# Performance work log

Measured on AMD Instinct MI355X. Metric: run time of the kernel, lower is better.

Reference implementation:

```python
import jax, jax.numpy as jnp
import numpy as np

B, S, D, H = 4, 2048, 256, 8
HD = D // H  # 32
SCALE = 1.0 / jnp.sqrt(256.0)  # module divides by sqrt(256.0), NOT sqrt(head_dim)


def setup_inputs() -> dict:
    key = jax.random.key(0)
    ks = jax.random.split(key, 11)
    inp = {
        "q_in": jax.random.normal(ks[0], (B, S, D), jnp.float32),
        "k_in": jax.random.normal(ks[1], (B, S, D), jnp.float32),
        "v_in": jax.random.normal(ks[2], (B, S, D), jnp.float32),
        # causal mask, broadcastable over batch and heads; every row has >=1 one
        "mask": jnp.tril(jnp.ones((S, S), jnp.float32))[None, None, :, :],
        "Wq": jax.random.normal(ks[3], (D, D), jnp.float32) * 0.05,
        "bq": jnp.zeros((D,), jnp.float32),
        "Wk": jax.random.normal(ks[4], (D, D), jnp.float32) * 0.05,
        "bk": jnp.zeros((D,), jnp.float32),
        "Wv": jax.random.normal(ks[5], (D, D), jnp.float32) * 0.05,
        "bv": jnp.zeros((D,), jnp.float32),
        "Wo": jax.random.normal(ks[6], (D, D), jnp.float32) * 0.05,
        "bo": jnp.zeros((D,), jnp.float32),
    }
    return inp


def _mask_softmax(x, mask):
    # faithful to module: exp (no max-subtraction), remask, normalize
    e = jnp.exp(x) * mask
    return e / jnp.sum(e, axis=-1, keepdims=True)


def reference(q_in, k_in, v_in, mask, Wq, bq, Wk, bk, Wv, bv, Wo, bo):
    Q = (q_in @ Wq + bq).reshape(B, S, H, HD)
    K = (k_in @ Wk + bk).reshape(B, S, H, HD)
    V = (v_in @ Wv + bv).reshape(B, S, H, HD)
    scores = jnp.einsum("bqhd,bkhd->bhqk", Q, K) * SCALE  # [B,H,S,S]
    scores = scores * mask  # module multiplies mask into scores first
    p = _mask_softmax(scores, mask)
    attn = jnp.einsum("bhqk,bkhd->bqhd", p, V).reshape(B, S, D)
    return attn @ Wo + bo
```

## Files before the change

kernel.cpp:

```cpp
#include <hip/hip_runtime.h>
#include <hip/hip_bf16.h>

#define BATCH 4
#define S_LEN 2048
#define D_MOD 256
#define NH 8
#define HDIM 32
#define SCALE_ 0.0625f

typedef short bf16x8 __attribute__((ext_vector_type(8)));
typedef short short4v __attribute__((ext_vector_type(4)));
typedef float f32x4 __attribute__((ext_vector_type(4)));

__device__ __forceinline__ short f2bf(float f) {
    __hip_bfloat16 h = __float2bfloat16(f);
    return *reinterpret_cast<short*>(&h);
}

__global__ __launch_bounds__(256) void wtrans_kernel(
    const float* __restrict__ Wq, const float* __restrict__ Wk,
    const float* __restrict__ Wv, const float* __restrict__ Wo,
    short* __restrict__ WT)
{
    const int wsel = blockIdx.x;
    const int k0 = blockIdx.y * 8;
    const float* W = wsel == 0 ? Wq : (wsel == 1 ? Wk : (wsel == 2 ? Wv : Wo));
    short* T = WT + (size_t)wsel * 256 * 256;
    int n = threadIdx.x;
    bf16x8 o;
    #pragma unroll
    for (int kk = 0; kk < 8; ++kk)
        o[kk] = f2bf(W[(size_t)(k0 + kk) * 256 + n]);
    *(bf16x8*)&T[(size_t)n * 256 + k0] = o;
}

__global__ __launch_bounds__(256) void qkv_proj_kernel(
    const float* __restrict__ q_in, const float* __restrict__ k_in,
    const float* __restrict__ v_in, const short* __restrict__ WT,
    const float* __restrict__ bq, const float* __restrict__ bk,
    const float* __restrict__ bv,
    short* __restrict__ Qp, short* __restrict__ Kp, short* __restrict__ Vt)
{
    __shared__ short lsA[32][264];
    const int mt = blockIdx.x;
    const int seg = blockIdx.y;
    const float* A = seg == 0 ? q_in : (seg == 1 ? k_in : v_in);
    const short* WTs = WT + (size_t)seg * 65536;
    const float* bias = seg == 0 ? bq : (seg == 1 ? bk : bv);
    const int m0 = mt * 32;
    const int tid = threadIdx.x;

    {
        const float4* A4 = (const float4*)(A + (size_t)m0 * D_MOD);
        #pragma unroll
        for (int i = 0; i < 8; ++i) {
            int f4 = tid + i * 256;
            int row = f4 >> 6, c4 = f4 & 63;
            float4 v = A4[f4];
            short4v o;
            o.x = f2bf(v.x); o.y = f2bf(v.y); o.z = f2bf(v.z); o.w = f2bf(v.w);
            *(short4v*)&lsA[row][c4 * 4] = o;
        }
    }
    __syncthreads();

    const int w = tid >> 6, l = tid & 63, g = l >> 4, r15 = l & 15;
    bf16x8 af[2][8];
    #pragma unroll
    for (int f = 0; f < 2; ++f)
        #pragma unroll
        for (int kk = 0; kk < 8; ++kk)
            af[f][kk] = *(const bf16x8*)&lsA[f * 16 + r15][kk * 32 + 8 * g];

    const int bidx = m0 >> 11;
    const int s_base = m0 & (S_LEN - 1);

    #pragma unroll
    for (int ntl = 0; ntl < 4; ++ntl) {
        int col = w * 64 + ntl * 16 + r15;
        f32x4 acc0 = {}, acc1 = {};
        #pragma unroll
        for (int kk = 0; kk < 8; ++kk) {
            bf16x8 b = *(const bf16x8*)&WTs[(size_t)col * 256 + kk * 32 + 8 * g];
            acc0 = __builtin_amdgcn_mfma_f32_16x16x32_bf16(af[0][kk], b, acc0, 0, 0, 0);
            acc1 = __builtin_amdgcn_mfma_f32_16x16x32_bf16(af[1][kk], b, acc1, 0, 0, 0);
        }
        float bval = bias[col];
        int h = col >> 5, hd = col & 31;
        if (seg < 2) {
            short* Out = seg == 0 ? Qp : Kp;
            short* Outh = Out + ((size_t)(bidx * NH + h) * S_LEN) * HDIM;
            #pragma unroll
            for (int r = 0; r < 4; ++r) {
                int s0 = s_base + 4 * g + r;
                Outh[(size_t)s0 * HDIM + hd]        = f2bf(acc0[r] + bval);
                Outh[(size_t)(s0 + 16) * HDIM + hd] = f2bf(acc1[r] + bval);
            }
        } else {
            short* Vh = Vt + ((size_t)(bidx * NH + h) * HDIM + hd) * S_LEN;
            short4v o0, o1;
            #pragma unroll
            for (int r = 0; r < 4; ++r) { o0[r] = f2bf(acc0[r] + bval); o1[r] = f2bf(acc1[r] + bval); }
            size_t s = s_base + 4 * g;
            *(short4v*)&Vh[s]      = o0;
            *(short4v*)&Vh[s + 16] = o1;
        }
    }
}

__global__ __launch_bounds__(256) void attn_kernel(
    const short* __restrict__ Qp, const short* __restrict__ Kp,
    const short* __restrict__ Vt, short* __restrict__ Ab)
{
    __shared__ char smem[18432];
    __shared__ float psl[4][2][16];
    short (*pl)[32][72] = (short(*)[32][72])smem;
    float (*comb)[32][33] = (float(*)[32][33])smem;

    const int idx = blockIdx.x;
    const int bh = 4 * (idx & 7) + ((idx >> 3) & 3);
    const int jq = idx >> 5;
    const int b = bh >> 3, h = bh & 7;
    const int tid = threadIdx.x;
    const int w = tid >> 6, l = tid & 63, g = l >> 4, r15 = l & 15;
    const int q0 = jq * 32;

    const short* Qph = Qp + (size_t)bh * S_LEN * HDIM;
    const short* Kph = Kp + (size_t)bh * S_LEN * HDIM;
    const short* Vtp = Vt + (size_t)bh * HDIM * S_LEN;

    bf16x8 aq0 = *(const bf16x8*)&Qph[(size_t)(q0 + r15) * HDIM + 8 * g];
    bf16x8 aq1 = *(const bf16x8*)&Qph[(size_t)(q0 + 16 + r15) * HDIM + 8 * g];

    f32x4 oacc[2][2] = {};
    float ps0[4] = {}, ps1[4] = {};
    const f32x4 zero = {};
    const int ntiles = (q0 + 95) >> 6;

    for (int kt = w; kt < ntiles; kt += 4) {
        const int k0 = kt * 64;
        const bool full = (k0 + 63) <= q0;
        #pragma unroll
        for (int n = 0; n < 4; ++n) {
            bf16x8 bk = *(const bf16x8*)&Kph[(size_t)(k0 + n * 16 + r15) * HDIM + 8 * g];
            f32x4 s0 = __builtin_amdgcn_mfma_f32_16x16x32_bf16(aq0, bk, zero, 0, 0, 0);
            f32x4 s1 = __builtin_amdgcn_mfma_f32_16x16x32_bf16(aq1, bk, zero, 0, 0, 0);
            int key = k0 + n * 16 + r15;
            if (full) {
                #pragma unroll
                for (int r = 0; r < 4; ++r) {
                    float e0 = __expf(s0[r] * SCALE_);
                    float e1 = __expf(s1[r] * SCALE_);
                    ps0[r] += e0; ps1[r] += e1;
                    pl[w][4 * g + r][n * 16 + r15]      = f2bf(e0);
                    pl[w][16 + 4 * g + r][n * 16 + r15] = f2bf(e1);
                }
            } else {
                #pragma unroll
                for (int r = 0; r < 4; ++r) {
                    int qr = q0 + 4 * g + r;
                    float e0 = (key <= qr)      ? __expf(s0[r] * SCALE_) : 0.0f;
                    float e1 = (key <= qr + 16) ? __expf(s1[r] * SCALE_) : 0.0f;
                    ps0[r] += e0; ps1[r] += e1;
                    pl[w][4 * g + r][n * 16 + r15]      = f2bf(e0);
                    pl[w][16 + 4 * g + r][n * 16 + r15] = f2bf(e1);
                }
            }
        }
        #pragma unroll
        for (int ks = 0; ks < 2; ++ks) {
            bf16x8 pa0 = *(const bf16x8*)&pl[w][r15][ks * 32 + 8 * g];
            bf16x8 pa1 = *(const bf16x8*)&pl[w][16 + r15][ks * 32 + 8 * g];
            #pragma unroll
            for (int n2 = 0; n2 < 2; ++n2) {
                bf16x8 bv = *(const bf16x8*)&Vtp[(size_t)(n2 * 16 + r15) * S_LEN + k0 + ks * 32 + 8 * g];
                oacc[0][n2] = __builtin_amdgcn_mfma_f32_16x16x32_bf16(pa0, bv, oacc[0][n2], 0, 0, 0);
                oacc[1][n2] = __builtin_amdgcn_mfma_f32_16x16x32_bf16(pa1, bv, oacc[1][n2], 0, 0, 0);
            }
        }
    }

    #pragma unroll
    for (int r = 0; r < 4; ++r) {
        float v0 = ps0[r], v1 = ps1[r];
        v0 += __shfl_xor(v0, 1); v1 += __shfl_xor(v1, 1);
        v0 += __shfl_xor(v0, 2); v1 += __shfl_xor(v1, 2);
        v0 += __shfl_xor(v0, 4); v1 += __shfl_xor(v1, 4);
        v0 += __shfl_xor(v0, 8); v1 += __shfl_xor(v1, 8);
        ps0[r] = v0; ps1[r] = v1;
    }

    __syncthreads();
    #pragma unroll
    for (int n2 = 0; n2 < 2; ++n2) {
        #pragma unroll
        for (int r = 0; r < 4; ++r) {
            comb[w][4 * g + r][n2 * 16 + r15]      = oacc[0][n2][r];
            comb[w][16 + 4 * g + r][n2 * 16 + r15] = oacc[1][n2][r];
        }
    }
    if (r15 == 0) {
        #pragma unroll
        for (int r = 0; r < 4; ++r) {
            psl[w][0][4 * g + r] = ps0[r];
            psl[w][1][4 * g + r] = ps1[r];
        }
    }
    __syncthreads();

    {
        int q = tid >> 3, hd0 = (tid & 7) * 4;
        int qf = q >> 4, q15 = q & 15;
        float ps = psl[0][qf][q15] + psl[1][qf][q15] + psl[2][qf][q15] + psl[3][qf][q15];
        float inv = __fdividef(1.0f, ps);
        short4v o;
        #pragma unroll
        for (int j = 0; j < 4; ++j) {
            float v = comb[0][q][hd0 + j] + comb[1][q][hd0 + j]
                    + comb[2][q][hd0 + j] + comb[3][q][hd0 + j];
            o[j] = f2bf(v * inv);
        }
        *(short4v*)&Ab[((size_t)b * S_LEN + q0 + q) * D_MOD + h * HDIM + hd0] = o;
    }
}

__global__ __launch_bounds__(256) void out_proj_kernel(
    const short* __restrict__ Ab, const short* __restrict__ WTo,
    const float* __restrict__ bo, float* __restrict__ out)
{
    const int m0 = blockIdx.x * 32;
    const int tid = threadIdx.x;
    const int w = tid >> 6, l = tid & 63, g = l >> 4, r15 = l & 15;

    bf16x8 af[2][8];
    #pragma unroll
    for (int f = 0; f < 2; ++f)
        #pragma unroll
        for (int kk = 0; kk < 8; ++kk)
            af[f][kk] = *(const bf16x8*)&Ab[(size_t)(m0 + f * 16 + r15) * D_MOD + kk * 32 + 8 * g];

    #pragma unroll
    for (int ntl = 0; ntl < 4; ++ntl) {
        int col = w * 64 + ntl * 16 + r15;
        f32x4 acc0 = {}, acc1 = {};
        #pragma unroll
        for (int kk = 0; kk < 8; ++kk) {
            bf16x8 bfr = *(const bf16x8*)&WTo[(size_t)col * 256 + kk * 32 + 8 * g];
            acc0 = __builtin_amdgcn_mfma_f32_16x16x32_bf16(af[0][kk], bfr, acc0, 0, 0, 0);
            acc1 = __builtin_amdgcn_mfma_f32_16x16x32_bf16(af[1][kk], bfr, acc1, 0, 0, 0);
        }
        float bval = bo[col];
        #pragma unroll
        for (int r = 0; r < 4; ++r) {
            out[(size_t)(m0 + 4 * g + r) * D_MOD + col]      = acc0[r] + bval;
            out[(size_t)(m0 + 16 + 4 * g + r) * D_MOD + col] = acc1[r] + bval;
        }
    }
}

extern "C" void kernel_launch(void* const* d_in, const int* in_sizes, int n_in,
                              void* d_out, int out_size, void* d_ws, size_t ws_size,
                              hipStream_t stream) {
    const float* q_in = (const float*)d_in[0];
    const float* k_in = (const float*)d_in[1];
    const float* v_in = (const float*)d_in[2];
    const float* Wq = (const float*)d_in[4];
    const float* bq = (const float*)d_in[5];
    const float* Wk = (const float*)d_in[6];
    const float* bk = (const float*)d_in[7];
    const float* Wv = (const float*)d_in[8];
    const float* bv = (const float*)d_in[9];
    const float* Wo = (const float*)d_in[10];
    const float* bo = (const float*)d_in[11];
    float* out = (float*)d_out;

    const size_t NTOK = (size_t)BATCH * S_LEN * D_MOD;
    short* WT = (short*)d_ws;
    short* Qp = WT + 4 * 65536;
    short* Kp = Qp + NTOK;
    short* Vt = Kp + NTOK;
    short* Ab = Vt + NTOK;

    wtrans_kernel<<<dim3(4, 32), 256, 0, stream>>>(Wq, Wk, Wv, Wo, WT);
    qkv_proj_kernel<<<dim3(256, 3), 256, 0, stream>>>(
        q_in, k_in, v_in, WT, bq, bk, bv, Qp, Kp, Vt);
    attn_kernel<<<2048, 256, 0, stream>>>(Qp, Kp, Vt, Ab);
    out_proj_kernel<<<256, 256, 0, stream>>>(Ab, WT + 3 * 65536, bo, out);
}
```

Baseline: 74.65 us.

## Prefetch next K tile into registers, reverse query-block order, add MFMA priority hints

Loads the K fragments for the next key tile one iteration ahead, so global-load latency overlaps the current tile's exp and PV MFMA work. Query blocks are launched in reverse order so the longest causal rows are scheduled first, aiming for better load balance across CUs. s_setprio raises wave priority around the MFMA sections. The costs are higher register pressure from the double-buffered K fragments, and possible scheduling side effects from the priority hints.

New measurement: 71.61 us. 1.04x faster.

```diff
diff --git a/kernel.cpp b/kernel.cpp
--- a/kernel.cpp
+++ b/kernel.cpp
@@ -119,7 +119,7 @@
 
     const int idx = blockIdx.x;
     const int bh = 4 * (idx & 7) + ((idx >> 3) & 3);
-    const int jq = idx >> 5;
+    const int jq = 63 - (idx >> 5);
     const int b = bh >> 3, h = bh & 7;
     const int tid = threadIdx.x;
     const int w = tid >> 6, l = tid & 63, g = l >> 4, r15 = l & 15;
@@ -137,20 +137,45 @@
     const f32x4 zero = {};
     const int ntiles = (q0 + 95) >> 6;
 
+    bf16x8 bkb[4];
+    {
+        const int k0 = w * 64;
+        if (w < ntiles) {
+            #pragma unroll
+            for (int n = 0; n < 4; ++n)
+                bkb[n] = *(const bf16x8*)&Kph[(size_t)(k0 + n * 16 + r15) * HDIM + 8 * g];
+        }
+    }
+
     for (int kt = w; kt < ntiles; kt += 4) {
         const int k0 = kt * 64;
         const bool full = (k0 + 63) <= q0;
+        bf16x8 bkn[4];
+        const int ktn = kt + 4;
+        if (ktn < ntiles) {
+            const int k0n = ktn * 64;
+            #pragma unroll
+            for (int n = 0; n < 4; ++n)
+                bkn[n] = *(const bf16x8*)&Kph[(size_t)(k0n + n * 16 + r15) * HDIM + 8 * g];
+        }
+
+        __builtin_amdgcn_s_setprio(1);
+        f32x4 s0v[4], s1v[4];
         #pragma unroll
         for (int n = 0; n < 4; ++n) {
-            bf16x8 bk = *(const bf16x8*)&Kph[(size_t)(k0 + n * 16 + r15) * HDIM + 8 * g];
-            f32x4 s0 = __builtin_amdgcn_mfma_f32_16x16x32_bf16(aq0, bk, zero, 0, 0, 0);
-            f32x4 s1 = __builtin_amdgcn_mfma_f32_16x16x32_bf16(aq1, bk, zero, 0, 0, 0);
+            s0v[n] = __builtin_amdgcn_mfma_f32_16x16x32_bf16(aq0, bkb[n], zero, 0, 0, 0);
+            s1v[n] = __builtin_amdgcn_mfma_f32_16x16x32_bf16(aq1, bkb[n], zero, 0, 0, 0);
+        }
+        __builtin_amdgcn_s_setprio(0);
+
+        #pragma unroll
+        for (int n = 0; n < 4; ++n) {
             int key = k0 + n * 16 + r15;
             if (full) {
                 #pragma unroll
                 for (int r = 0; r < 4; ++r) {
-                    float e0 = __expf(s0[r] * SCALE_);
-                    float e1 = __expf(s1[r] * SCALE_);
+                    float e0 = __expf(s0v[n][r] * SCALE_);
+                    float e1 = __expf(s1v[n][r] * SCALE_);
                     ps0[r] += e0; ps1[r] += e1;
                     pl[w][4 * g + r][n * 16 + r15]      = f2bf(e0);
                     pl[w][16 + 4 * g + r][n * 16 + r15] = f2bf(e1);
@@ -159,14 +184,16 @@
                 #pragma unroll
                 for (int r = 0; r < 4; ++r) {
                     int qr = q0 + 4 * g + r;
-                    float e0 = (key <= qr)      ? __expf(s0[r] * SCALE_) : 0.0f;
-                    float e1 = (key <= qr + 16) ? __expf(s1[r] * SCALE_) : 0.0f;
+                    float e0 = (key <= qr)      ? __expf(s0v[n][r] * SCALE_) : 0.0f;
+                    float e1 = (key <= qr + 16) ? __expf(s1v[n][r] * SCALE_) : 0.0f;
                     ps0[r] += e0; ps1[r] += e1;
                     pl[w][4 * g + r][n * 16 + r15]      = f2bf(e0);
                     pl[w][16 + 4 * g + r][n * 16 + r15] = f2bf(e1);
                 }
             }
         }
+
+        __builtin_amdgcn_s_setprio(1);
         #pragma unroll
         for (int ks = 0; ks < 2; ++ks) {
             bf16x8 pa0 = *(const bf16x8*)&pl[w][r15][ks * 32 + 8 * g];
@@ -177,6 +204,12 @@
                 oacc[0][n2] = __builtin_amdgcn_mfma_f32_16x16x32_bf16(pa0, bv, oacc[0][n2], 0, 0, 0);
                 oacc[1][n2] = __builtin_amdgcn_mfma_f32_16x16x32_bf16(pa1, bv, oacc[1][n2], 0, 0, 0);
             }
+        }
+        __builtin_amdgcn_s_setprio(0);
+
+        if (ktn < ntiles) {
+            #pragma unroll
+            for (int n = 0; n < 4; ++n) bkb[n] = bkn[n];
         }
     }
 
```

## Keep attention probabilities in registers via transposed QK MFMA, prescale Q by log2e

Applied to the files above, without the earlier changes.

The QK^T MFMA now runs with swapped operands, so the score tile comes out transposed and its exp values can feed the PV MFMA directly from registers. This removes the per-wave LDS round trip for P and the shared buffer it needed. Q is pre-multiplied by scale*log2(e) in the projection kernel so the attention loop can use exp2f. The change also launches the longest causal query blocks first, issues V loads at the top of each tile, and raises wave priority around MFMAs. Keys are re-permuted to match the register layout, which makes the ordering of keys and V rows subtle to get right.

New measurement: 87.78 us. 1.18x slower.

```diff
diff --git a/kernel.cpp b/kernel.cpp
--- a/kernel.cpp
+++ b/kernel.cpp
@@ -6,7 +6,7 @@
 #define D_MOD 256
 #define NH 8
 #define HDIM 32
-#define SCALE_ 0.0625f
+#define QLOG2E 0.09016844f
 
 typedef short bf16x8 __attribute__((ext_vector_type(8)));
 typedef short short4v __attribute__((ext_vector_type(4)));
@@ -87,9 +87,16 @@
         }
         float bval = bias[col];
         int h = col >> 5, hd = col & 31;
-        if (seg < 2) {
-            short* Out = seg == 0 ? Qp : Kp;
-            short* Outh = Out + ((size_t)(bidx * NH + h) * S_LEN) * HDIM;
+        if (seg == 0) {
+            short* Outh = Qp + ((size_t)(bidx * NH + h) * S_LEN) * HDIM;
+            #pragma unroll
+            for (int r = 0; r < 4; ++r) {
+                int s0 = s_base + 4 * g + r;
+                Outh[(size_t)s0 * HDIM + hd]        = f2bf((acc0[r] + bval) * QLOG2E);
+                Outh[(size_t)(s0 + 16) * HDIM + hd] = f2bf((acc1[r] + bval) * QLOG2E);
+            }
+        } else if (seg == 1) {
+            short* Outh = Kp + ((size_t)(bidx * NH + h) * S_LEN) * HDIM;
             #pragma unroll
             for (int r = 0; r < 4; ++r) {
                 int s0 = s_base + 4 * g + r;
@@ -112,15 +119,13 @@
     const short* __restrict__ Qp, const short* __restrict__ Kp,
     const short* __restrict__ Vt, short* __restrict__ Ab)
 {
-    __shared__ char smem[18432];
+    __shared__ float comb[4][32][36];
     __shared__ float psl[4][2][16];
-    short (*pl)[32][72] = (short(*)[32][72])smem;
-    float (*comb)[32][33] = (float(*)[32][33])smem;
 
     const int idx = blockIdx.x;
     const int bh = 4 * (idx & 7) + ((idx >> 3) & 3);
-    const int jq = idx >> 5;
-    const int b = bh >> 3, h = bh & 7;
+    const int jq = 63 - (idx >> 5);
+    const int b = bh >> 3, hh = bh & 7;
     const int tid = threadIdx.x;
     const int w = tid >> 6, l = tid & 63, g = l >> 4, r15 = l & 15;
     const int q0 = jq * 32;
@@ -129,89 +134,100 @@
     const short* Kph = Kp + (size_t)bh * S_LEN * HDIM;
     const short* Vtp = Vt + (size_t)bh * HDIM * S_LEN;
 
-    bf16x8 aq0 = *(const bf16x8*)&Qph[(size_t)(q0 + r15) * HDIM + 8 * g];
-    bf16x8 aq1 = *(const bf16x8*)&Qph[(size_t)(q0 + 16 + r15) * HDIM + 8 * g];
-
-    f32x4 oacc[2][2] = {};
-    float ps0[4] = {}, ps1[4] = {};
+    bf16x8 aq0 = *(const bf16x8*)&Qph[(q0 + r15) * HDIM + 8 * g];
+    bf16x8 aq1 = *(const bf16x8*)&Qph[(q0 + 16 + r15) * HDIM + 8 * g];
+
+    f32x4 o00 = {}, o01 = {}, o10 = {}, o11 = {};
+    float ps0 = 0.f, ps1 = 0.f;
     const f32x4 zero = {};
     const int ntiles = (q0 + 95) >> 6;
 
-    for (int kt = w; kt < ntiles; kt += 4) {
+    const short* kp  = Kph + w * 2048 + r15 * 32 + 8 * g;
+    const short* vp0 = Vtp + r15 * S_LEN + w * 64 + 4 * g;
+    const short* vp1 = vp0 + 16 * S_LEN;
+
+    for (int kt = w; kt < ntiles; kt += 4, kp += 8192, vp0 += 256, vp1 += 256) {
         const int k0 = kt * 64;
         const bool full = (k0 + 63) <= q0;
+
+        short4v v000 = *(const short4v*)(vp0);
+        short4v v001 = *(const short4v*)(vp0 + 16);
+        short4v v010 = *(const short4v*)(vp1);
+        short4v v011 = *(const short4v*)(vp1 + 16);
+        short4v v100 = *(const short4v*)(vp0 + 32);
+        short4v v101 = *(const short4v*)(vp0 + 48);
+        short4v v110 = *(const short4v*)(vp1 + 32);
+        short4v v111 = *(const short4v*)(vp1 + 48);
+
+        short4v pb[4][2];
         #pragma unroll
         for (int n = 0; n < 4; ++n) {
-            bf16x8 bk = *(const bf16x8*)&Kph[(size_t)(k0 + n * 16 + r15) * HDIM + 8 * g];
-            f32x4 s0 = __builtin_amdgcn_mfma_f32_16x16x32_bf16(aq0, bk, zero, 0, 0, 0);
-            f32x4 s1 = __builtin_amdgcn_mfma_f32_16x16x32_bf16(aq1, bk, zero, 0, 0, 0);
-            int key = k0 + n * 16 + r15;
+            bf16x8 ak = *(const bf16x8*)(kp + n * 512);
+            __builtin_amdgcn_s_setprio(1);
+            f32x4 s0 = __builtin_amdgcn_mfma_f32_16x16x32_bf16(ak, aq0, zero, 0, 0, 0);
+            f32x4 s1 = __builtin_amdgcn_mfma_f32_16x16x32_bf16(ak, aq1, zero, 0, 0, 0);
+            __builtin_amdgcn_s_setprio(0);
             if (full) {
                 #pragma unroll
                 for (int r = 0; r < 4; ++r) {
-                    float e0 = __expf(s0[r] * SCALE_);
-                    float e1 = __expf(s1[r] * SCALE_);
-                    ps0[r] += e0; ps1[r] += e1;
-                    pl[w][4 * g + r][n * 16 + r15]      = f2bf(e0);
-                    pl[w][16 + 4 * g + r][n * 16 + r15] = f2bf(e1);
+                    float e0 = exp2f(s0[r]);
+                    float e1 = exp2f(s1[r]);
+                    ps0 += e0; ps1 += e1;
+                    pb[n][0][r] = f2bf(e0);
+                    pb[n][1][r] = f2bf(e1);
                 }
             } else {
+                const int kb = k0 + n * 16 + 4 * g;
                 #pragma unroll
                 for (int r = 0; r < 4; ++r) {
-                    int qr = q0 + 4 * g + r;
-                    float e0 = (key <= qr)      ? __expf(s0[r] * SCALE_) : 0.0f;
-                    float e1 = (key <= qr + 16) ? __expf(s1[r] * SCALE_) : 0.0f;
-                    ps0[r] += e0; ps1[r] += e1;
-                    pl[w][4 * g + r][n * 16 + r15]      = f2bf(e0);
-                    pl[w][16 + 4 * g + r][n * 16 + r15] = f2bf(e1);
+                    int key = kb + r;
+                    float e0 = (key <= q0 + r15)      ? exp2f(s0[r]) : 0.0f;
+                    float e1 = (key <= q0 + 16 + r15) ? exp2f(s1[r]) : 0.0f;
+                    ps0 += e0; ps1 += e1;
+                    pb[n][0][r] = f2bf(e0);
+                    pb[n][1][r] = f2bf(e1);
                 }
             }
         }
-        #pragma unroll
-        for (int ks = 0; ks < 2; ++ks) {
-            bf16x8 pa0 = *(const bf16x8*)&pl[w][r15][ks * 32 + 8 * g];
-            bf16x8 pa1 = *(const bf16x8*)&pl[w][16 + r15][ks * 32 + 8 * g];
-            #pragma unroll
-            for (int n2 = 0; n2 < 2; ++n2) {
-                bf16x8 bv = *(const bf16x8*)&Vtp[(size_t)(n2 * 16 + r15) * S_LEN + k0 + ks * 32 + 8 * g];
-                oacc[0][n2] = __builtin_amdgcn_mfma_f32_16x16x32_bf16(pa0, bv, oacc[0][n2], 0, 0, 0);
-                oacc[1][n2] = __builtin_amdgcn_mfma_f32_16x16x32_bf16(pa1, bv, oacc[1][n2], 0, 0, 0);
-            }
-        }
-    }
-
+
+        bf16x8 pa00 = __builtin_shufflevector(pb[0][0], pb[1][0], 0,1,2,3,4,5,6,7);
+        bf16x8 pa01 = __builtin_shufflevector(pb[0][1], pb[1][1], 0,1,2,3,4,5,6,7);
+        bf16x8 pa10 = __builtin_shufflevector(pb[2][0], pb[3][0], 0,1,2,3,4,5,6,7);
+        bf16x8 pa11 = __builtin_shufflevector(pb[2][1], pb[3][1], 0,1,2,3,4,5,6,7);
+        bf16x8 bv00 = __builtin_shufflevector(v000, v001, 0,1,2,3,4,5,6,7);
+        bf16x8 bv01 = __builtin_shufflevector(v010, v011, 0,1,2,3,4,5,6,7);
+        bf16x8 bv10 = __builtin_shufflevector(v100, v101, 0,1,2,3,4,5,6,7);
+        bf16x8 bv11 = __builtin_shufflevector(v110, v111, 0,1,2,3,4,5,6,7);
+
+        __builtin_amdgcn_s_setprio(1);
+        o00 = __builtin_amdgcn_mfma_f32_16x16x32_bf16(pa00, bv00, o00, 0, 0, 0);
+        o01 = __builtin_amdgcn_mfma_f32_16x16x32_bf16(pa00, bv01, o01, 0, 0, 0);
+        o10 = __builtin_amdgcn_mfma_f32_16x16x32_bf16(pa01, bv00, o10, 0, 0, 0);
+        o11 = __builtin_amdgcn_mfma_f32_16x16x32_bf16(pa01, bv01, o11, 0, 0, 0);
+        o00 = __builtin_amdgcn_mfma_f32_16x16x32_bf16(pa10, bv10, o00, 0, 0, 0);
+        o01 = __builtin_amdgcn_mfma_f32_16x16x32_bf16(pa10, bv11, o01, 0, 0, 0);
+        o10 = __builtin_amdgcn_mfma_f32_16x16x32_bf16(pa11, bv10, o10, 0, 0, 0);
+        o11 = __builtin_amdgcn_mfma_f32_16x16x32_bf16(pa11, bv11, o11, 0, 0, 0);
+        __builtin_amdgcn_s_setprio(0);
+    }
+
+    ps0 += __shfl_xor(ps0, 16); ps0 += __shfl_xor(ps0, 32);
+    ps1 += __shfl_xor(ps1, 16); ps1 += __shfl_xor(ps1, 32);
+
+    if (l < 16) { psl[w][0][l] = ps0; psl[w][1][l] = ps1; }
     #pragma unroll
     for (int r = 0; r < 4; ++r) {
-        float v0 = ps0[r], v1 = ps1[r];
-        v0 += __shfl_xor(v0, 1); v1 += __shfl_xor(v1, 1);
-        v0 += __shfl_xor(v0, 2); v1 += __shfl_xor(v1, 2);
-        v0 += __shfl_xor(v0, 4); v1 += __shfl_xor(v1, 4);
-        v0 += __shfl_xor(v0, 8); v1 += __shfl_xor(v1, 8);
-        ps0[r] = v0; ps1[r] = v1;
-    }
-
-    __syncthreads();
-    #pragma unroll
-    for (int n2 = 0; n2 < 2; ++n2) {
-        #pragma unroll
-        for (int r = 0; r < 4; ++r) {
-            comb[w][4 * g + r][n2 * 16 + r15]      = oacc[0][n2][r];
-            comb[w][16 + 4 * g + r][n2 * 16 + r15] = oacc[1][n2][r];
-        }
-    }
-    if (r15 == 0) {
-        #pragma unroll
-        for (int r = 0; r < 4; ++r) {
-            psl[w][0][4 * g + r] = ps0[r];
-            psl[w][1][4 * g + r] = ps1[r];
-        }
+        comb[w][4 * g + r][r15]           = o00[r];
+        comb[w][4 * g + r][16 + r15]      = o01[r];
+        comb[w][16 + 4 * g + r][r15]      = o10[r];
+        comb[w][16 + 4 * g + r][16 + r15] = o11[r];
     }
     __syncthreads();
 
     {
         int q = tid >> 3, hd0 = (tid & 7) * 4;
-        int qf = q >> 4, q15 = q & 15;
-        float ps = psl[0][qf][q15] + psl[1][qf][q15] + psl[2][qf][q15] + psl[3][qf][q15];
+        float ps = psl[0][q >> 4][q & 15] + psl[1][q >> 4][q & 15]
+                 + psl[2][q >> 4][q & 15] + psl[3][q >> 4][q & 15];
         float inv = __fdividef(1.0f, ps);
         short4v o;
         #pragma unroll
@@ -220,7 +236,7 @@
                     + comb[2][q][hd0 + j] + comb[3][q][hd0 + j];
             o[j] = f2bf(v * inv);
         }
-        *(short4v*)&Ab[((size_t)b * S_LEN + q0 + q) * D_MOD + h * HDIM + hd0] = o;
+        *(short4v*)&Ab[((size_t)b * S_LEN + q0 + q) * D_MOD + hh * HDIM + hd0] = o;
     }
 }
 
```
